# Optimization experiments

Hardware: AMD Instinct MI355X
Metric: run time of the kernel (lower is better)

Reference implementation:

```python
import jax, jax.numpy as jnp
import numpy as np

# --- config constants (match init_kwargs) ---
TOP_K = 2          # num_experts_per_token
N_GROUP = 4        # num_expert_group
TOPK_GROUP = 2     # groups selected per token
SCALE = 2.5        # routed_scaling_factor
B, S, D = 2, 2048, 1024
E, F = 8, 512      # num_experts, moe_intermediate_size
SH = 1024          # shared intermediate = moe_intermediate_size * num_shared_experts


def setup_inputs() -> dict:
    key = jax.random.key(0)
    ks = jax.random.split(key, 10)
    w = 0.02
    return {
        "hidden_states": jax.random.normal(ks[0], (B, S, D), jnp.float32),
        "gate_w": jax.random.normal(ks[1], (E, D), jnp.float32) * w,
        "gate_bias": jax.random.normal(ks[2], (E,), jnp.float32) * 0.01,
        "w1": jax.random.normal(ks[3], (E, F, D), jnp.float32) * w,
        "w2": jax.random.normal(ks[4], (E, D, F), jnp.float32) * w,
        "w3": jax.random.normal(ks[5], (E, F, D), jnp.float32) * w,
        "shared_gate_w": jax.random.normal(ks[6], (SH, D), jnp.float32) * w,
        "shared_up_w": jax.random.normal(ks[7], (SH, D), jnp.float32) * w,
        "shared_down_w": jax.random.normal(ks[8], (D, SH), jnp.float32) * w,
    }


def _moe_gate(x2d, gate_w, gate_bias):
    """DeepSeek-V3 style group-limited sigmoid gate (inference path)."""
    T = x2d.shape[0]
    logits = x2d.astype(jnp.float32) @ gate_w.T.astype(jnp.float32)  # [T,E]
    scores = jax.nn.sigmoid(logits)
    sc = scores + gate_bias[None, :]                                  # e_score_correction_bias
    grp = sc.reshape(T, N_GROUP, E // N_GROUP)
    group_scores = jax.lax.top_k(grp, 2)[0].sum(-1)                   # [T,G] sum of top-2 in group
    gidx = jax.lax.top_k(group_scores, TOPK_GROUP)[1]                 # [T,topk_group]
    gmask = jnp.zeros((T, N_GROUP), sc.dtype).at[jnp.arange(T)[:, None], gidx].set(1.0)
    smask = jnp.repeat(gmask, E // N_GROUP, axis=1)                   # [T,E]
    tmp = jnp.where(smask > 0, sc, 0.0)                               # masked_fill(~mask, 0)
    tidx = jax.lax.top_k(tmp, TOP_K)[1]                               # [T,top_k]
    tw = jnp.take_along_axis(scores, tidx, axis=1)                    # weights from unbiased scores
    tw = tw / (tw.sum(-1, keepdims=True) + 1e-20)                     # moe_renormalize
    return tidx, tw * SCALE


def reference(hidden_states, gate_w, gate_bias, w1, w2, w3,
              shared_gate_w, shared_up_w, shared_down_w):
    b, s, d = hidden_states.shape
    x = hidden_states.reshape(-1, d)                                  # [T,D]
    T = x.shape[0]
    tidx, tw = _moe_gate(x, gate_w, gate_bias)
    # dense combine weights: ew[t,e] = sum_k tw[t,k] * (tidx[t,k]==e)
    ew = jnp.zeros((T, E), x.dtype).at[jnp.arange(T)[:, None], tidx].add(tw.astype(x.dtype))
    # routed experts (SwiGLU), computed per expert and combined with ew
    h = jax.nn.silu(jnp.einsum('td,efd->tef', x, w1)) * jnp.einsum('td,efd->tef', x, w3)
    y = jnp.einsum('tef,edf,te->td', h, w2, ew)
    # shared experts applied to identity
    shared = (jax.nn.silu(x @ shared_gate_w.T) * (x @ shared_up_w.T)) @ shared_down_w.T
    return (y + shared).reshape(b, s, d)
```

## Files before the change

kernel.cpp:

```cpp
#include <hip/hip_runtime.h>
#include <hip/hip_bf16.h>
#include <stdint.h>

#define T_TOK 4096
#define D_DIM 1024
#define E_NUM 8
#define F_DIM 512
#define SH_DIM 1024
#define SCALE_F 2.5f

#define BM 128
#define BN 128
#define BK 32
#define TILE_E (BM * BK)

#define NBIG (E_NUM * F_DIM * D_DIM)
#define NSML (SH_DIM * D_DIM)
#define NCONV_CHUNKS ((3 * NBIG + 3 * NSML) / 4)
#define MAX_TILES 72

#define UP_SHARED_BLOCKS 256
#define UP_TOTAL (UP_SHARED_BLOCKS + MAX_TILES * 4)
#define DN_SHARED_BLOCKS 256
#define DN_TOTAL (DN_SHARED_BLOCKS + MAX_TILES * 8)

typedef unsigned short ushort_t;
typedef __attribute__((ext_vector_type(8))) short short8;
typedef __attribute__((ext_vector_type(4))) short short4v;
typedef __attribute__((ext_vector_type(4))) float f32x4;

#define GLL16(g, l)                                                                  \
  __builtin_amdgcn_global_load_lds(                                                  \
      (const __attribute__((address_space(1))) void*)(g),                            \
      (__attribute__((address_space(3))) void*)(l), 16, 0, 0)

#define WAIT_VM(N) asm volatile("s_waitcnt vmcnt(" #N ")" ::: "memory")
#define CFENCE()   asm volatile("" ::: "memory")

__device__ inline ushort_t f2bf(float f) {
  union { float f; unsigned u; } cv; cv.f = f;
  unsigned u = cv.u;
  unsigned r = (u + 0x7FFFu + ((u >> 16) & 1u)) >> 16;
  return (ushort_t)r;
}

__global__ void gate_kernel(const float* __restrict__ x, const float* __restrict__ gw,
                            const float* __restrict__ gb, float* __restrict__ ew,
                            ushort_t* __restrict__ xb) {
  int t = blockIdx.x;
  int lane = threadIdx.x;
  const float* xr = x + (size_t)t * D_DIM;
  float xv[16];
#pragma unroll
  for (int i = 0; i < 16; i++) xv[i] = xr[lane + (i << 6)];
#pragma unroll
  for (int i = 0; i < 16; i++) xb[(size_t)t * D_DIM + lane + (i << 6)] = f2bf(xv[i]);
  float logit[E_NUM];
#pragma unroll
  for (int e = 0; e < E_NUM; e++) {
    const float* wr = gw + (size_t)e * D_DIM;
    float s = 0.f;
#pragma unroll
    for (int i = 0; i < 16; i++) s += xv[i] * wr[lane + (i << 6)];
#pragma unroll
    for (int off = 32; off; off >>= 1) s += __shfl_xor(s, off, 64);
    logit[e] = s;
  }
  if (lane == 0) {
    float scores[E_NUM], sc[E_NUM];
#pragma unroll
    for (int e = 0; e < E_NUM; e++) {
      scores[e] = 1.f / (1.f + expf(-logit[e]));
      sc[e] = scores[e] + gb[e];
    }
    float gs[4];
#pragma unroll
    for (int g = 0; g < 4; g++) gs[g] = sc[2 * g] + sc[2 * g + 1];
    int g0 = 0;
#pragma unroll
    for (int g = 1; g < 4; g++) if (gs[g] > gs[g0]) g0 = g;
    int g1 = -1;
#pragma unroll
    for (int g = 0; g < 4; g++) { if (g == g0) continue; if (g1 < 0 || gs[g] > gs[g1]) g1 = g; }
    float tmp[E_NUM];
#pragma unroll
    for (int e = 0; e < E_NUM; e++) {
      int g = e >> 1;
      tmp[e] = (g == g0 || g == g1) ? sc[e] : 0.f;
    }
    int e0 = 0;
#pragma unroll
    for (int e = 1; e < E_NUM; e++) if (tmp[e] > tmp[e0]) e0 = e;
    int e1 = -1;
#pragma unroll
    for (int e = 0; e < E_NUM; e++) { if (e == e0) continue; if (e1 < 0 || tmp[e] > tmp[e1]) e1 = e; }
    float w0 = scores[e0], w1v = scores[e1];
    float inv = SCALE_F / (w0 + w1v + 1e-20f);
    float o[E_NUM];
#pragma unroll
    for (int e = 0; e < E_NUM; e++) o[e] = 0.f;
    o[e0] = w0 * inv;
    o[e1] = w1v * inv;
#pragma unroll
    for (int e = 0; e < E_NUM; e++) ew[t * E_NUM + e] = o[e];
  }
}

__global__ void convert_kernel(const float* __restrict__ w1, const float* __restrict__ w2,
                               const float* __restrict__ w3, const float* __restrict__ sg,
                               const float* __restrict__ su, const float* __restrict__ sd,
                               ushort_t* __restrict__ w1b, ushort_t* __restrict__ w2b,
                               ushort_t* __restrict__ w3b, ushort_t* __restrict__ sgb,
                               ushort_t* __restrict__ sub, ushort_t* __restrict__ sdb) {
  size_t chunk = (size_t)blockIdx.x * blockDim.x + threadIdx.x;
  if (chunk >= (size_t)NCONV_CHUNKS) return;
  size_t idx = chunk * 4;
  const float* src; ushort_t* dst;
  if (idx < (size_t)NBIG)                    { src = w1; dst = w1b; }
  else if (idx < 2ull * NBIG)                { src = w2; dst = w2b; idx -= (size_t)NBIG; }
  else if (idx < 3ull * NBIG)                { src = w3; dst = w3b; idx -= 2ull * NBIG; }
  else if (idx < 3ull * NBIG + NSML)         { src = sg; dst = sgb; idx -= 3ull * NBIG; }
  else if (idx < 3ull * NBIG + 2ull * NSML)  { src = su; dst = sub; idx -= 3ull * NBIG + NSML; }
  else                                       { src = sd; dst = sdb; idx -= 3ull * NBIG + 2ull * NSML; }
  f32x4 v = *(const f32x4*)&src[idx];
  short4v o;
  o[0] = (short)f2bf(v[0]); o[1] = (short)f2bf(v[1]);
  o[2] = (short)f2bf(v[2]); o[3] = (short)f2bf(v[3]);
  *(short4v*)&dst[idx] = o;
}

__global__ void build_lists(const float* __restrict__ ew, int* __restrict__ counts,
                            int* __restrict__ toklist) {
  int t = blockIdx.x * blockDim.x + threadIdx.x;
  if (t >= T_TOK) return;
#pragma unroll
  for (int e = 0; e < E_NUM; e++) {
    if (ew[t * E_NUM + e] > 0.f) {
      int p = atomicAdd(&counts[e], 1);
      toklist[e * T_TOK + p] = t;
    }
  }
}

__global__ void assign_kernel(const int* __restrict__ counts, int4* __restrict__ assign,
                              int* __restrict__ meta) {
  if (threadIdx.x != 0 || blockIdx.x != 0) return;
  int total = 0, base = 0;
  for (int e = 0; e < E_NUM; e++) {
    int c = counts[e];
    int nt = (c + BM - 1) / BM;
    for (int i = 0; i < nt; i++) {
      assign[total] = make_int4(e, i, base, c);
      total++;
    }
    base += nt * BM;
  }
  meta[0] = total;
}

__global__ __launch_bounds__(256, 2)
void up_gemm(const ushort_t* __restrict__ xb,
             const ushort_t* __restrict__ sgb, const ushort_t* __restrict__ sub,
             const ushort_t* __restrict__ w1b, const ushort_t* __restrict__ w3b,
             const int* __restrict__ toklist,
             const int4* __restrict__ assign, const int* __restrict__ meta,
             ushort_t* __restrict__ hsh, ushort_t* __restrict__ hbuf) {
  __shared__ ushort_t la[3 * TILE_E], lb1[3 * TILE_E], lb2[3 * TILE_E];
  __shared__ int ttok[BM];
  int bid = blockIdx.x;
  int tid = threadIdx.x, wid = tid >> 6, lane = tid & 63;

  const ushort_t *b1base, *b2base;
  ushort_t* dst;
  int n0, dstride;
  size_t rowbase;

  if (bid < UP_SHARED_BLOCKS) {
    int m0 = (bid >> 3) * BM;
    n0 = (bid & 7) * BN;
    b1base = sgb + (size_t)n0 * D_DIM;
    b2base = sub + (size_t)n0 * D_DIM;
    dst = hsh; dstride = SH_DIM; rowbase = m0;
    if (tid < BM) ttok[tid] = m0 + tid;
  } else {
    int rid = bid - UP_SHARED_BLOCKS;
    int tidx = rid >> 2;
    if (tidx >= meta[0]) return;
    int4 as = assign[tidx];
    int e = as.x, tile = as.y, sbase = as.z, cnt = as.w;
    n0 = (rid & 3) * BN;
    b1base = w1b + ((size_t)e * F_DIM + n0) * D_DIM;
    b2base = w3b + ((size_t)e * F_DIM + n0) * D_DIM;
    dst = hbuf; dstride = F_DIM; rowbase = (size_t)sbase + (size_t)tile * BM;
    if (tid < BM) {
      int idx = tile * BM + tid;
      ttok[tid] = (idx < cnt) ? toklist[e * T_TOK + idx] : -1;
    }
  }
  __syncthreads();

  int srow = (wid << 5) + (lane >> 2);
  int c16 = lane & 3;
  int s0 = c16 ^ ((srow >> 1) & 3);
  int s1 = c16 ^ (((srow + 16) >> 1) & 3);
  int tka = ttok[srow], tkb = ttok[srow + 16];
  const ushort_t* gA0 = xb + (size_t)(tka < 0 ? 0 : tka) * D_DIM + (s0 << 3);
  const ushort_t* gA1 = xb + (size_t)(tkb < 0 ? 0 : tkb) * D_DIM + (s1 << 3);
  const ushort_t* gB1a = b1base + (size_t)srow * D_DIM + (s0 << 3);
  const ushort_t* gB1b = b1base + (size_t)(srow + 16) * D_DIM + (s1 << 3);
  const ushort_t* gB2a = b2base + (size_t)srow * D_DIM + (s0 << 3);
  const ushort_t* gB2b = b2base + (size_t)(srow + 16) * D_DIM + (s1 << 3);
  int wo0 = (wid << 10);
  int wo1 = (wid << 10) + 512;

  int wm = (wid >> 1) << 6, wn = (wid & 1) << 6;
  int rsel = lane & 15, g = lane >> 4;
  int offA[4], offB[4];
#pragma unroll
  for (int i = 0; i < 4; i++) {
    int R = wm + i * 16 + rsel;
    offA[i] = (R << 5) + ((g ^ ((R >> 1) & 3)) << 3);
    int R2 = wn + i * 16 + rsel;
    offB[i] = (R2 << 5) + ((g ^ ((R2 >> 1) & 3)) << 3);
  }

  f32x4 acc1[4][4] = {{{0.f}}}, acc2[4][4] = {{{0.f}}};

  GLL16(gA0, la + wo0);   GLL16(gA1, la + wo1);
  GLL16(gB1a, lb1 + wo0); GLL16(gB1b, lb1 + wo1);
  GLL16(gB2a, lb2 + wo0); GLL16(gB2b, lb2 + wo1);
  gA0 += BK; gA1 += BK; gB1a += BK; gB1b += BK; gB2a += BK; gB2b += BK;

  const int NT = D_DIM / BK;
  int cur = 0;
  for (int t = 0; t < NT; ++t) {
    int nb = cur + 1; if (nb == 3) nb = 0;
    int nbase = nb * TILE_E;
    if (t + 1 < NT) {
      GLL16(gA0, la + nbase + wo0);   GLL16(gA1, la + nbase + wo1);
      GLL16(gB1a, lb1 + nbase + wo0); GLL16(gB1b, lb1 + nbase + wo1);
      GLL16(gB2a, lb2 + nbase + wo0); GLL16(gB2b, lb2 + nbase + wo1);
      gA0 += BK; gA1 += BK; gB1a += BK; gB1b += BK; gB2a += BK; gB2b += BK;
      WAIT_VM(6);
    } else {
      WAIT_VM(0);
    }
    __builtin_amdgcn_s_barrier();
    CFENCE();
    int base = cur * TILE_E;
    short8 af[4], bf1[4], bf2[4];
#pragma unroll
    for (int i = 0; i < 4; i++) {
      af[i]  = *(const short8*)&la[base + offA[i]];
      bf1[i] = *(const short8*)&lb1[base + offB[i]];
      bf2[i] = *(const short8*)&lb2[base + offB[i]];
    }
#pragma unroll
    for (int mi = 0; mi < 4; mi++)
#pragma unroll
      for (int ni = 0; ni < 4; ni++) {
        acc1[mi][ni] = __builtin_amdgcn_mfma_f32_16x16x32_bf16(af[mi], bf1[ni], acc1[mi][ni], 0, 0, 0);
        acc2[mi][ni] = __builtin_amdgcn_mfma_f32_16x16x32_bf16(af[mi], bf2[ni], acc2[mi][ni], 0, 0, 0);
      }
    CFENCE();
    cur = nb;
  }

  int cw = lane & 15, rw = (lane >> 4) << 2;
#pragma unroll
  for (int mi = 0; mi < 4; mi++)
#pragma unroll
    for (int ni = 0; ni < 4; ni++)
#pragma unroll
      for (int r = 0; r < 4; r++) {
        int lrow = wm + mi * 16 + rw + r;
        int col = n0 + wn + ni * 16 + cw;
        float gg = acc1[mi][ni][r], u = acc2[mi][ni][r];
        float h = gg * (1.f / (1.f + __expf(-gg))) * u;
        dst[(rowbase + lrow) * (size_t)dstride + col] = f2bf(h);
      }
}

__global__ __launch_bounds__(256, 2)
void down_gemm(const ushort_t* __restrict__ hsh, const ushort_t* __restrict__ hbuf,
               const ushort_t* __restrict__ sdb, const ushort_t* __restrict__ w2b,
               const int* __restrict__ toklist, const float* __restrict__ ew,
               const int4* __restrict__ assign, const int* __restrict__ meta,
               float* __restrict__ out) {
  __shared__ ushort_t la[3 * TILE_E], lb[3 * TILE_E];
  __shared__ int ttok[BM];
  __shared__ float twt[BM];
  int bid = blockIdx.x;
  int tid = threadIdx.x, wid = tid >> 6, lane = tid & 63;

  const ushort_t *abase, *bbase;
  int n0, kend;

  if (bid < DN_SHARED_BLOCKS) {
    int m0 = (bid >> 3) * BM;
    n0 = (bid & 7) * BN;
    abase = hsh + (size_t)m0 * SH_DIM;
    bbase = sdb + (size_t)n0 * SH_DIM;
    kend = SH_DIM;
    if (tid < BM) { ttok[tid] = m0 + tid; twt[tid] = 1.f; }
  } else {
    int rid = bid - DN_SHARED_BLOCKS;
    int tidx = rid >> 3;
    if (tidx >= meta[0]) return;
    int4 as = assign[tidx];
    int e = as.x, tile = as.y, sbase = as.z, cnt = as.w;
    n0 = (rid & 7) * BN;
    abase = hbuf + ((size_t)sbase + (size_t)tile * BM) * F_DIM;
    bbase = w2b + ((size_t)e * D_DIM + n0) * F_DIM;
    kend = F_DIM;
    if (tid < BM) {
      int idx = tile * BM + tid;
      int tk = (idx < cnt) ? toklist[e * T_TOK + idx] : -1;
      ttok[tid] = tk;
      twt[tid] = (tk >= 0) ? ew[tk * E_NUM + e] : 0.f;
    }
  }
  __syncthreads();

  int srow = (wid << 5) + (lane >> 2);
  int c16 = lane & 3;
  int s0 = c16 ^ ((srow >> 1) & 3);
  int s1 = c16 ^ (((srow + 16) >> 1) & 3);
  const ushort_t* gA0 = abase + (size_t)srow * kend + (s0 << 3);
  const ushort_t* gA1 = abase + (size_t)(srow + 16) * kend + (s1 << 3);
  const ushort_t* gB0 = bbase + (size_t)srow * kend + (s0 << 3);
  const ushort_t* gB1 = bbase + (size_t)(srow + 16) * kend + (s1 << 3);
  int wo0 = (wid << 10);
  int wo1 = (wid << 10) + 512;

  int wm = (wid >> 1) << 6, wn = (wid & 1) << 6;
  int rsel = lane & 15, g = lane >> 4;
  int offA[4], offB[4];
#pragma unroll
  for (int i = 0; i < 4; i++) {
    int R = wm + i * 16 + rsel;
    offA[i] = (R << 5) + ((g ^ ((R >> 1) & 3)) << 3);
    int R2 = wn + i * 16 + rsel;
    offB[i] = (R2 << 5) + ((g ^ ((R2 >> 1) & 3)) << 3);
  }

  f32x4 acc[4][4] = {{{0.f}}};

  GLL16(gA0, la + wo0); GLL16(gA1, la + wo1);
  GLL16(gB0, lb + wo0); GLL16(gB1, lb + wo1);
  gA0 += BK; gA1 += BK; gB0 += BK; gB1 += BK;

  const int NT = kend / BK;
  int cur = 0;
  for (int t = 0; t < NT; ++t) {
    int nb = cur + 1; if (nb == 3) nb = 0;
    int nbase = nb * TILE_E;
    if (t + 1 < NT) {
      GLL16(gA0, la + nbase + wo0); GLL16(gA1, la + nbase + wo1);
      GLL16(gB0, lb + nbase + wo0); GLL16(gB1, lb + nbase + wo1);
      gA0 += BK; gA1 += BK; gB0 += BK; gB1 += BK;
      WAIT_VM(4);
    } else {
      WAIT_VM(0);
    }
    __builtin_amdgcn_s_barrier();
    CFENCE();
    int base = cur * TILE_E;
    short8 af[4], bf[4];
#pragma unroll
    for (int i = 0; i < 4; i++) {
      af[i] = *(const short8*)&la[base + offA[i]];
      bf[i] = *(const short8*)&lb[base + offB[i]];
    }
#pragma unroll
    for (int mi = 0; mi < 4; mi++)
#pragma unroll
      for (int ni = 0; ni < 4; ni++)
        acc[mi][ni] = __builtin_amdgcn_mfma_f32_16x16x32_bf16(af[mi], bf[ni], acc[mi][ni], 0, 0, 0);
    CFENCE();
    cur = nb;
  }

  int cw = lane & 15, rw = (lane >> 4) << 2;
#pragma unroll
  for (int mi = 0; mi < 4; mi++)
#pragma unroll
    for (int ni = 0; ni < 4; ni++)
#pragma unroll
      for (int r = 0; r < 4; r++) {
        int lrow = wm + mi * 16 + rw + r;
        int tk = ttok[lrow];
        if (tk >= 0) {
          int col = n0 + wn + ni * 16 + cw;
          atomicAdd(&out[(size_t)tk * D_DIM + col], twt[lrow] * acc[mi][ni][r]);
        }
      }
}

extern "C" void kernel_launch(void* const* d_in, const int* in_sizes, int n_in,
                              void* d_out, int out_size, void* d_ws, size_t ws_size,
                              hipStream_t stream) {
  const float* x  = (const float*)d_in[0];
  const float* gw = (const float*)d_in[1];
  const float* gb = (const float*)d_in[2];
  const float* w1 = (const float*)d_in[3];
  const float* w2 = (const float*)d_in[4];
  const float* w3 = (const float*)d_in[5];
  const float* sg = (const float*)d_in[6];
  const float* su = (const float*)d_in[7];
  const float* sd = (const float*)d_in[8];
  float* out = (float*)d_out;

  char* ws = (char*)d_ws;
  size_t off = 0;
  auto alloc = [&](size_t bytes) {
    char* p = ws + off;
    off += (bytes + 255) & ~(size_t)255;
    return p;
  };
  ushort_t* xb   = (ushort_t*)alloc((size_t)T_TOK * D_DIM * 2);
  ushort_t* w1b  = (ushort_t*)alloc((size_t)NBIG * 2);
  ushort_t* w2b  = (ushort_t*)alloc((size_t)NBIG * 2);
  ushort_t* w3b  = (ushort_t*)alloc((size_t)NBIG * 2);
  ushort_t* sgb  = (ushort_t*)alloc((size_t)NSML * 2);
  ushort_t* sub  = (ushort_t*)alloc((size_t)NSML * 2);
  ushort_t* sdb  = (ushort_t*)alloc((size_t)NSML * 2);
  float*    ew   = (float*)alloc((size_t)T_TOK * E_NUM * 4);
  ushort_t* hsh  = (ushort_t*)alloc((size_t)T_TOK * SH_DIM * 2);
  ushort_t* hbuf = (ushort_t*)alloc((size_t)MAX_TILES * BM * F_DIM * 2);
  int*      toklist = (int*)alloc((size_t)E_NUM * T_TOK * 4);
  int*      counts  = (int*)alloc(64);
  int4*     assign  = (int4*)alloc((MAX_TILES + 8) * sizeof(int4));
  int*      meta    = (int*)alloc(64);

  hipMemsetAsync(counts, 0, 64, stream);
  hipMemsetAsync(out, 0, (size_t)out_size * sizeof(float), stream);
  gate_kernel<<<T_TOK, 64, 0, stream>>>(x, gw, gb, ew, xb);
  convert_kernel<<<NCONV_CHUNKS / 256, 256, 0, stream>>>(w1, w2, w3, sg, su, sd,
                                                         w1b, w2b, w3b, sgb, sub, sdb);
  build_lists<<<(T_TOK + 255) / 256, 256, 0, stream>>>(ew, counts, toklist);
  assign_kernel<<<1, 64, 0, stream>>>(counts, assign, meta);
  up_gemm<<<UP_TOTAL, 256, 0, stream>>>(xb, sgb, sub, w1b, w3b, toklist, assign, meta,
                                        hsh, hbuf);
  down_gemm<<<DN_TOTAL, 256, 0, stream>>>(hsh, hbuf, sdb, w2b, toklist, ew, assign, meta,
                                          out);
}
```

Measured before the change: 276.5 us.

## Deepen GEMM prefetch to two stages, fuse list building and output zeroing

The up and down GEMM main loops now prefetch two K-tiles ahead into the three-buffer LDS ring, issuing the next load after the barrier so more global-to-LDS traffic is in flight during MFMA work. Token-list construction moves into the gate kernel, which removes the separate build_lists launch. Zeroing of the output moves into the weight conversion kernel, which removes a memset. The down GEMM launch bound is raised to three blocks per CU, which may cost registers and cause spills.

```diff
diff --git a/kernel.cpp b/kernel.cpp
--- a/kernel.cpp
+++ b/kernel.cpp
@@ -17,6 +17,7 @@
 #define NBIG (E_NUM * F_DIM * D_DIM)
 #define NSML (SH_DIM * D_DIM)
 #define NCONV_CHUNKS ((3 * NBIG + 3 * NSML) / 4)
+#define NOUT_CHUNKS (T_TOK * D_DIM / 4)
 #define MAX_TILES 72
 
 #define UP_SHARED_BLOCKS 256
@@ -46,7 +47,8 @@
 
 __global__ void gate_kernel(const float* __restrict__ x, const float* __restrict__ gw,
                             const float* __restrict__ gb, float* __restrict__ ew,
-                            ushort_t* __restrict__ xb) {
+                            ushort_t* __restrict__ xb, int* __restrict__ counts,
+                            int* __restrict__ toklist) {
   int t = blockIdx.x;
   int lane = threadIdx.x;
   const float* xr = x + (size_t)t * D_DIM;
@@ -103,6 +105,10 @@
     o[e1] = w1v * inv;
 #pragma unroll
     for (int e = 0; e < E_NUM; e++) ew[t * E_NUM + e] = o[e];
+    int p0 = atomicAdd(&counts[e0], 1);
+    toklist[e0 * T_TOK + p0] = t;
+    int p1 = atomicAdd(&counts[e1], 1);
+    toklist[e1 * T_TOK + p1] = t;
   }
 }
 
@@ -111,9 +117,16 @@
                                const float* __restrict__ su, const float* __restrict__ sd,
                                ushort_t* __restrict__ w1b, ushort_t* __restrict__ w2b,
                                ushort_t* __restrict__ w3b, ushort_t* __restrict__ sgb,
-                               ushort_t* __restrict__ sub, ushort_t* __restrict__ sdb) {
+                               ushort_t* __restrict__ sub, ushort_t* __restrict__ sdb,
+                               float* __restrict__ outz) {
   size_t chunk = (size_t)blockIdx.x * blockDim.x + threadIdx.x;
-  if (chunk >= (size_t)NCONV_CHUNKS) return;
+  if (chunk >= (size_t)(NCONV_CHUNKS + NOUT_CHUNKS)) return;
+  if (chunk >= (size_t)NCONV_CHUNKS) {
+    size_t oi = (chunk - NCONV_CHUNKS) * 4;
+    f32x4 z = {0.f, 0.f, 0.f, 0.f};
+    *(f32x4*)&outz[oi] = z;
+    return;
+  }
   size_t idx = chunk * 4;
   const float* src; ushort_t* dst;
   if (idx < (size_t)NBIG)                    { src = w1; dst = w1b; }
@@ -127,19 +140,6 @@
   o[0] = (short)f2bf(v[0]); o[1] = (short)f2bf(v[1]);
   o[2] = (short)f2bf(v[2]); o[3] = (short)f2bf(v[3]);
   *(short4v*)&dst[idx] = o;
-}
-
-__global__ void build_lists(const float* __restrict__ ew, int* __restrict__ counts,
-                            int* __restrict__ toklist) {
-  int t = blockIdx.x * blockDim.x + threadIdx.x;
-  if (t >= T_TOK) return;
-#pragma unroll
-  for (int e = 0; e < E_NUM; e++) {
-    if (ew[t * E_NUM + e] > 0.f) {
-      int p = atomicAdd(&counts[e], 1);
-      toklist[e * T_TOK + p] = t;
-    }
-  }
 }
 
 __global__ void assign_kernel(const int* __restrict__ counts, int4* __restrict__ assign,
@@ -226,27 +226,29 @@
 
   f32x4 acc1[4][4] = {{{0.f}}}, acc2[4][4] = {{{0.f}}};
 
-  GLL16(gA0, la + wo0);   GLL16(gA1, la + wo1);
-  GLL16(gB1a, lb1 + wo0); GLL16(gB1b, lb1 + wo1);
-  GLL16(gB2a, lb2 + wo0); GLL16(gB2b, lb2 + wo1);
-  gA0 += BK; gA1 += BK; gB1a += BK; gB1b += BK; gB2a += BK; gB2b += BK;
+#pragma unroll
+  for (int p = 0; p < 2; p++) {
+    int pb = p * TILE_E;
+    GLL16(gA0, la + pb + wo0);   GLL16(gA1, la + pb + wo1);
+    GLL16(gB1a, lb1 + pb + wo0); GLL16(gB1b, lb1 + pb + wo1);
+    GLL16(gB2a, lb2 + pb + wo0); GLL16(gB2b, lb2 + pb + wo1);
+    gA0 += BK; gA1 += BK; gB1a += BK; gB1b += BK; gB2a += BK; gB2b += BK;
+  }
 
   const int NT = D_DIM / BK;
   int cur = 0;
   for (int t = 0; t < NT; ++t) {
-    int nb = cur + 1; if (nb == 3) nb = 0;
-    int nbase = nb * TILE_E;
-    if (t + 1 < NT) {
+    if (t < NT - 1) { WAIT_VM(6); } else { WAIT_VM(0); }
+    __builtin_amdgcn_s_barrier();
+    CFENCE();
+    if (t + 2 < NT) {
+      int nb = cur + 2; if (nb >= 3) nb -= 3;
+      int nbase = nb * TILE_E;
       GLL16(gA0, la + nbase + wo0);   GLL16(gA1, la + nbase + wo1);
       GLL16(gB1a, lb1 + nbase + wo0); GLL16(gB1b, lb1 + nbase + wo1);
       GLL16(gB2a, lb2 + nbase + wo0); GLL16(gB2b, lb2 + nbase + wo1);
       gA0 += BK; gA1 += BK; gB1a += BK; gB1b += BK; gB2a += BK; gB2b += BK;
-      WAIT_VM(6);
-    } else {
-      WAIT_VM(0);
-    }
-    __builtin_amdgcn_s_barrier();
-    CFENCE();
+    }
     int base = cur * TILE_E;
     short8 af[4], bf1[4], bf2[4];
 #pragma unroll
@@ -263,7 +265,7 @@
         acc2[mi][ni] = __builtin_amdgcn_mfma_f32_16x16x32_bf16(af[mi], bf2[ni], acc2[mi][ni], 0, 0, 0);
       }
     CFENCE();
-    cur = nb;
+    cur = cur + 1; if (cur == 3) cur = 0;
   }
 
   int cw = lane & 15, rw = (lane >> 4) << 2;
@@ -281,7 +283,7 @@
       }
 }
 
-__global__ __launch_bounds__(256, 2)
+__global__ __launch_bounds__(256, 3)
 void down_gemm(const ushort_t* __restrict__ hsh, const ushort_t* __restrict__ hbuf,
                const ushort_t* __restrict__ sdb, const ushort_t* __restrict__ w2b,
                const int* __restrict__ toklist, const float* __restrict__ ew,
@@ -346,25 +348,27 @@
 
   f32x4 acc[4][4] = {{{0.f}}};
 
-  GLL16(gA0, la + wo0); GLL16(gA1, la + wo1);
-  GLL16(gB0, lb + wo0); GLL16(gB1, lb + wo1);
-  gA0 += BK; gA1 += BK; gB0 += BK; gB1 += BK;
+#pragma unroll
+  for (int p = 0; p < 2; p++) {
+    int pb = p * TILE_E;
+    GLL16(gA0, la + pb + wo0); GLL16(gA1, la + pb + wo1);
+    GLL16(gB0, lb + pb + wo0); GLL16(gB1, lb + pb + wo1);
+    gA0 += BK; gA1 += BK; gB0 += BK; gB1 += BK;
+  }
 
   const int NT = kend / BK;
   int cur = 0;
   for (int t = 0; t < NT; ++t) {
-    int nb = cur + 1; if (nb == 3) nb = 0;
-    int nbase = nb * TILE_E;
-    if (t + 1 < NT) {
+    if (t < NT - 1) { WAIT_VM(4); } else { WAIT_VM(0); }
+    __builtin_amdgcn_s_barrier();
+    CFENCE();
+    if (t + 2 < NT) {
+      int nb = cur + 2; if (nb >= 3) nb -= 3;
+      int nbase = nb * TILE_E;
       GLL16(gA0, la + nbase + wo0); GLL16(gA1, la + nbase + wo1);
       GLL16(gB0, lb + nbase + wo0); GLL16(gB1, lb + nbase + wo1);
       gA0 += BK; gA1 += BK; gB0 += BK; gB1 += BK;
-      WAIT_VM(4);
-    } else {
-      WAIT_VM(0);
-    }
-    __builtin_amdgcn_s_barrier();
-    CFENCE();
+    }
     int base = cur * TILE_E;
     short8 af[4], bf[4];
 #pragma unroll
@@ -378,7 +382,7 @@
       for (int ni = 0; ni < 4; ni++)
         acc[mi][ni] = __builtin_amdgcn_mfma_f32_16x16x32_bf16(af[mi], bf[ni], acc[mi][ni], 0, 0, 0);
     CFENCE();
-    cur = nb;
+    cur = cur + 1; if (cur == 3) cur = 0;
   }
 
   int cw = lane & 15, rw = (lane >> 4) << 2;
@@ -434,11 +438,9 @@
   int*      meta    = (int*)alloc(64);
 
   hipMemsetAsync(counts, 0, 64, stream);
-  hipMemsetAsync(out, 0, (size_t)out_size * sizeof(float), stream);
-  gate_kernel<<<T_TOK, 64, 0, stream>>>(x, gw, gb, ew, xb);
-  convert_kernel<<<NCONV_CHUNKS / 256, 256, 0, stream>>>(w1, w2, w3, sg, su, sd,
-                                                         w1b, w2b, w3b, sgb, sub, sdb);
-  build_lists<<<(T_TOK + 255) / 256, 256, 0, stream>>>(ew, counts, toklist);
+  gate_kernel<<<T_TOK, 64, 0, stream>>>(x, gw, gb, ew, xb, counts, toklist);
+  convert_kernel<<<(NCONV_CHUNKS + NOUT_CHUNKS) / 256, 256, 0, stream>>>(
+      w1, w2, w3, sg, su, sd, w1b, w2b, w3b, sgb, sub, sdb, out);
   assign_kernel<<<1, 64, 0, stream>>>(counts, assign, meta);
   up_gemm<<<UP_TOTAL, 256, 0, stream>>>(xb, sgb, sub, w1b, w3b, toklist, assign, meta,
                                         hsh, hbuf);
```

Result: slower. 375.7 us (+35.9%).
